# Optimization experiments

Hardware: AMD Instinct MI355X
Metric: run time of the kernel (lower is better)

## Reference

```python
import jax, jax.numpy as jnp
import numpy as np

B, N, FIN, HID, HEADS, LAYERS = 2048, 62, 128, 512, 8, 3
FOUT = HID // HEADS  # 64


def setup_inputs() -> dict:
    key = jax.random.key(0)
    ks = jax.random.split(key, 12)
    x = jax.random.normal(ks[0], (B, N, FIN), dtype=jnp.float32)
    adj = jax.random.randint(ks[1], (B, N, N), 0, 2, dtype=jnp.int32)
    # BatchNorm1d(62) params (eval mode, running stats)
    bn_gamma = jax.random.normal(ks[2], (N,), dtype=jnp.float32) * 0.1 + 1.0
    bn_beta = jax.random.normal(ks[3], (N,), dtype=jnp.float32) * 0.1
    bn_mean = jax.random.normal(ks[4], (N,), dtype=jnp.float32) * 0.1
    bn_var = jax.random.uniform(ks[5], (N,), dtype=jnp.float32, minval=0.5, maxval=1.5)
    # input MLP
    W_mlp = jax.random.normal(ks[6], (FIN, HID), dtype=jnp.float32) / np.sqrt(FIN)
    b_mlp = jnp.zeros((HID,), dtype=jnp.float32)
    # GAT params: one W [HID, FOUT] and one a [2*FOUT] per (layer, head)
    W_gat = jax.random.normal(ks[7], (LAYERS, HEADS, HID, FOUT), dtype=jnp.float32) / np.sqrt(HID)
    a_gat = jax.random.normal(ks[8], (LAYERS, HEADS, 2 * FOUT), dtype=jnp.float32) / np.sqrt(2 * FOUT)
    # output head
    W_out = jax.random.normal(ks[9], (HID, 3), dtype=jnp.float32) / np.sqrt(HID)
    b_out = jnp.zeros((3,), dtype=jnp.float32)
    return {
        "x": x, "adj": adj,
        "bn_gamma": bn_gamma, "bn_beta": bn_beta, "bn_mean": bn_mean, "bn_var": bn_var,
        "W_mlp": W_mlp, "b_mlp": b_mlp,
        "W_gat": W_gat, "a_gat": a_gat,
        "W_out": W_out, "b_out": b_out,
    }


def reference(x, adj, bn_gamma, bn_beta, bn_mean, bn_var, W_mlp, b_mlp, W_gat, a_gat, W_out, b_out):
    eps = 1e-5
    alpha = 0.2  # LeakyReLU slope
    # BatchNorm1d over the node dim (C=62), eval mode
    xb = (x - bn_mean[None, :, None]) * (bn_gamma / jnp.sqrt(bn_var + eps))[None, :, None] + bn_beta[None, :, None]
    h_x = xb @ W_mlp + b_mlp  # [B, N, HID]
    mask = adj > 0  # [B, N, N]
    n_layers, n_heads, _, f_out = W_gat.shape
    for l in range(n_layers):
        # all heads at once: h [H, B, N, FOUT]
        h = jnp.einsum('bnf,hfd->hbnd', h_x, W_gat[l])
        a1 = a_gat[l][:, :f_out]   # multiplies the repeat(1,N,1) part -> h_j
        a2 = a_gat[l][:, f_out:]   # multiplies the repeat(1,1,N) part -> h_i
        f1 = jnp.einsum('hbnd,hd->hbn', h, a1)  # per-node source term
        f2 = jnp.einsum('hbnd,hd->hbn', h, a2)  # per-node dest term
        # e[h,b,i,j] = leaky(a2.h_i + a1.h_j)  (matches cat/repeat layout)
        e = jax.nn.leaky_relu(f2[:, :, :, None] + f1[:, :, None, :], alpha)
        e = jnp.where(mask[None], e, jnp.float32(-9e15))
        # torch F.softmax(attention, dim=1) on [B,N,N] -> axis=2 here (the i axis)
        att = jax.nn.softmax(e, axis=2)
        hp = jnp.einsum('hbij,hbjd->hbid', att, h)
        hp = jax.nn.elu(hp)
        # concat heads on feature dim -> [B, N, HID]
        h_x = jnp.transpose(hp, (1, 2, 0, 3)).reshape(h_x.shape[0], h_x.shape[1], n_heads * f_out)
    pooled = jnp.sum(h_x, axis=1)  # [B, HID]
    logits = pooled @ W_out + b_out  # [B, 3]
    return jax.nn.log_softmax(logits, axis=-1)
```

## Files before the change

### kernel.cpp

```cpp
#include <hip/hip_runtime.h>
#include <cstdint>
#include <cstddef>

#define B_ 2048
#define N_ 62
#define FIN_ 128
#define HID_ 512
#define HEADS_ 8
#define FOUT_ 64
#define LAYERS_ 3
#define M_ (B_*N_)

typedef __bf16 bf16x8 __attribute__((ext_vector_type(8)));
typedef __bf16 bf16x4 __attribute__((ext_vector_type(4)));
typedef float  f32x4  __attribute__((ext_vector_type(4)));
typedef unsigned short u16;

#define LOG2E 1.4426950408889634f

#if __has_builtin(__builtin_amdgcn_exp2f)
#define EXP2F(x) __builtin_amdgcn_exp2f(x)
#else
#define EXP2F(x) exp2f(x)
#endif
#if __has_builtin(__builtin_amdgcn_logf)
#define LOG2F(x) __builtin_amdgcn_logf(x)
#else
#define LOG2F(x) log2f(x)
#endif

static __device__ __forceinline__ u16 f2bf(float f) {
    union { float f; uint32_t u; } v; v.f = f;
    uint32_t u = v.u;
    return (u16)((u + 0x7fffu + ((u >> 16) & 1u)) >> 16);
}
static __device__ __forceinline__ float bf2f(u16 s) {
    union { uint32_t u; float f; } v; v.u = ((uint32_t)s) << 16;
    return v.f;
}
static __device__ __forceinline__ float rdlane(float v, int l) {
    union { float f; int i; } a, b; a.f = v;
    b.i = __builtin_amdgcn_readlane(a.i, l);
    return b.f;
}
static __device__ __forceinline__ bf16x4 pack4(f32x4 v) {
    bf16x4 o;
    o[0] = (__bf16)v[0]; o[1] = (__bf16)v[1];
    o[2] = (__bf16)v[2]; o[3] = (__bf16)v[3];
    return o;
}

__global__ __launch_bounds__(256) void repack_w(
    const float* __restrict__ Wm, const float* __restrict__ Wg,
    u16* __restrict__ wmlp_t, u16* __restrict__ wgat2)
{
    int idx = blockIdx.x * 256 + threadIdx.x;
    const int T1 = HID_ * FIN_;
    const int T2 = LAYERS_ * HEADS_ * 64 * HID_;
    if (idx < T1) {
        int n = idx / FIN_, k = idx % FIN_;
        wmlp_t[idx] = f2bf(Wm[k * HID_ + n]);
    } else if (idx < T1 + T2) {
        int j = idx - T1;
        int lh = j / (64 * HID_);
        int r  = j % (64 * HID_);
        int n = r / HID_, k = r % HID_;
        wgat2[j] = f2bf(Wg[((size_t)lh * HID_ + k) * FOUT_ + n]);
    }
}

__global__ __launch_bounds__(256) void build_masks(
    const int* __restrict__ adj, uint64_t* __restrict__ masks,
    uint64_t* __restrict__ masksT)
{
    __shared__ uint32_t m32[128];
    const int b = blockIdx.x, tid = threadIdx.x;
    if (tid < 128) m32[tid] = 0;
    __syncthreads();
    const int* a = adj + (size_t)b * N_ * N_;
    for (int idx = tid; idx < N_ * N_; idx += 256) {
        int i = idx / N_, j = idx % N_;
        if (a[idx] > 0) atomicOr(&m32[i * 2 + (j >> 5)], 1u << (j & 31));
    }
    __syncthreads();
    if (tid < 128) ((uint32_t*)(masks + (size_t)b * 64))[tid] = m32[tid];
    if (tid < 64) {
        int j = tid;
        uint64_t c = 0;
        for (int i = 0; i < N_; i++) {
            uint64_t bit = (m32[i * 2 + (j >> 5)] >> (j & 31)) & 1u;
            c |= bit << i;
        }
        masksT[(size_t)b * 64 + j] = c;
    }
}

#define S_R  72
#define RSZ  4608
#define S_X  136
#define X0   27648

__global__ __launch_bounds__(512, 4) void gat_fused(
    const float* __restrict__ x,
    const float* __restrict__ bng, const float* __restrict__ bnb,
    const float* __restrict__ bnm, const float* __restrict__ bnv,
    const u16* __restrict__ wmlp_t, const float* __restrict__ bm,
    const u16* __restrict__ wgat2, const float* __restrict__ ag,
    const uint64_t* __restrict__ masks, const uint64_t* __restrict__ masksT,
    const float* __restrict__ Wout, const float* __restrict__ bout,
    float* __restrict__ out)
{
    __shared__ __align__(16) u16 buf[36864];
    __shared__ uint64_t msk[64];
    __shared__ __align__(16) float fstat[1544];
    float* F1 = fstat;
    float* F2 = fstat + 512;
    float* LS = fstat + 1024;

    const int tid = threadIdx.x, b = blockIdx.x;
    const int wave = tid >> 6, lane = tid & 63;
    const int lr = lane & 15, lq = lane >> 4;
    const int w64 = wave * 64;
    const int wreg = wave * RSZ;

    const uint64_t cm = masksT[(size_t)b * 64 + lane];
    const uint32_t cml = (uint32_t)cm, cmh = (uint32_t)(cm >> 32);

    {
        const float* xg = x + (size_t)b * N_ * FIN_;
        for (int idx = tid; idx < 2048; idx += 512) {
            int n = idx >> 5, kq = idx & 31;
            bf16x4 o = {(__bf16)0.f, (__bf16)0.f, (__bf16)0.f, (__bf16)0.f};
            if (n < N_) {
                float s = bng[n] * rsqrtf(bnv[n] + 1e-5f);
                float sh = bnb[n] - bnm[n] * s;
                float4 v = *(const float4*)(xg + n * FIN_ + kq * 4);
                o[0] = (__bf16)(v.x * s + sh); o[1] = (__bf16)(v.y * s + sh);
                o[2] = (__bf16)(v.z * s + sh); o[3] = (__bf16)(v.w * s + sh);
            }
            *(bf16x4*)&buf[X0 + n * S_X + kq * 4] = o;
        }
        if (tid < 64) msk[tid] = (tid < N_) ? masks[(size_t)b * 64 + tid] : 0ull;
    }
    __syncthreads();

    {
        f32x4 acc[4][4];
#pragma unroll
        for (int mt = 0; mt < 4; mt++)
#pragma unroll
            for (int nt = 0; nt < 4; nt++) acc[mt][nt] = (f32x4){0.f, 0.f, 0.f, 0.f};
        const int c0 = w64;
#pragma unroll 1
        for (int kt = 0; kt < 4; kt++) {
            int k0 = kt * 32;
            bf16x8 xf[4];
#pragma unroll
            for (int nt = 0; nt < 4; nt++)
                xf[nt] = *(const bf16x8*)&buf[X0 + (nt * 16 + lr) * S_X + k0 + lq * 8];
#pragma unroll
            for (int mt = 0; mt < 4; mt++) {
                bf16x8 wf = *(const bf16x8*)(wmlp_t + (size_t)(c0 + mt * 16 + lr) * FIN_ + k0 + lq * 8);
#pragma unroll
                for (int nt = 0; nt < 4; nt++)
                    acc[mt][nt] = __builtin_amdgcn_mfma_f32_16x16x32_bf16(
                        wf, xf[nt], acc[mt][nt], 0, 0, 0);
            }
        }
        __syncthreads();
        f32x4 bl[4];
#pragma unroll
        for (int mt = 0; mt < 4; mt++)
            bl[mt] = *(const f32x4*)&bm[c0 + mt * 16 + lq * 4];
#pragma unroll
        for (int mt = 0; mt < 4; mt++)
#pragma unroll
            for (int nt = 0; nt < 4; nt++) {
                int node = nt * 16 + lr;
                *(bf16x4*)&buf[wreg + node * S_R + mt * 16 + lq * 4] =
                    pack4(acc[mt][nt] + bl[mt]);
            }
        if (lane < 16) {
            uint4 z = {0u, 0u, 0u, 0u};
            *(uint4*)&buf[wreg + (N_ + (lane >> 3)) * S_R + (lane & 7) * 8] = z;
        }
    }
    __syncthreads();

#pragma unroll 1
    for (int l = 0; l < LAYERS_; l++) {
        const u16* wp = wgat2 + (size_t)(l * HEADS_ + wave) * 64 * HID_;

        f32x4 acc[4][4];
#pragma unroll
        for (int mt = 0; mt < 4; mt++)
#pragma unroll
            for (int nt = 0; nt < 4; nt++) acc[mt][nt] = (f32x4){0.f, 0.f, 0.f, 0.f};
#pragma unroll 1
        for (int kt = 0; kt < 16; kt++) {
            int koff = (kt >> 1) * RSZ + (kt & 1) * 32 + lq * 8;
            bf16x8 af[4];
#pragma unroll
            for (int mt = 0; mt < 4; mt++)
                af[mt] = *(const bf16x8*)&buf[koff + (mt * 16 + lr) * S_R];
#pragma unroll
            for (int nt = 0; nt < 4; nt++) {
                bf16x8 bfr = *(const bf16x8*)(wp + (size_t)(nt * 16 + lr) * HID_ + kt * 32 + lq * 8);
#pragma unroll
                for (int mt = 0; mt < 4; mt++)
                    acc[mt][nt] = __builtin_amdgcn_mfma_f32_16x16x32_bf16(
                        af[mt], bfr, acc[mt][nt], 0, 0, 0);
            }
        }

        {
            float a1v[4], a2v[4];
            const float* agl = ag + (size_t)(l * HEADS_ + wave) * 128;
#pragma unroll
            for (int nt = 0; nt < 4; nt++) {
                a1v[nt] = agl[nt * 16 + lr] * LOG2E;
                a2v[nt] = agl[64 + nt * 16 + lr] * LOG2E;
            }
            float p1v[16], p2v[16];
#pragma unroll
            for (int mt = 0; mt < 4; mt++)
#pragma unroll
                for (int r = 0; r < 4; r++) {
                    float s1 = 0.f, s2 = 0.f;
#pragma unroll
                    for (int nt = 0; nt < 4; nt++) {
                        float hv = acc[mt][nt][r];
                        s1 = fmaf(hv, a1v[nt], s1);
                        s2 = fmaf(hv, a2v[nt], s2);
                    }
                    p1v[mt * 4 + r] = s1;
                    p2v[mt * 4 + r] = s2;
                }
#pragma unroll
            for (int c = 0; c < 8; c++) {
                float tA = __shfl_xor(p1v[c], 8, 64);
                float tB = __shfl_xor(p1v[c + 8], 8, 64);
                p1v[c] = (lr & 8) ? (p1v[c + 8] + tB) : (p1v[c] + tA);
                float uA = __shfl_xor(p2v[c], 8, 64);
                float uB = __shfl_xor(p2v[c + 8], 8, 64);
                p2v[c] = (lr & 8) ? (p2v[c + 8] + uB) : (p2v[c] + uA);
            }
#pragma unroll
            for (int c = 0; c < 4; c++) {
                float tA = __shfl_xor(p1v[c], 4, 64);
                float tB = __shfl_xor(p1v[c + 4], 4, 64);
                p1v[c] = (lr & 4) ? (p1v[c + 4] + tB) : (p1v[c] + tA);
                float uA = __shfl_xor(p2v[c], 4, 64);
                float uB = __shfl_xor(p2v[c + 4], 4, 64);
                p2v[c] = (lr & 4) ? (p2v[c + 4] + uB) : (p2v[c] + uA);
            }
#pragma unroll
            for (int c = 0; c < 2; c++) {
                float tA = __shfl_xor(p1v[c], 2, 64);
                float tB = __shfl_xor(p1v[c + 2], 2, 64);
                p1v[c] = (lr & 2) ? (p1v[c + 2] + tB) : (p1v[c] + tA);
                float uA = __shfl_xor(p2v[c], 2, 64);
                float uB = __shfl_xor(p2v[c + 2], 2, 64);
                p2v[c] = (lr & 2) ? (p2v[c + 2] + uB) : (p2v[c] + uA);
            }
            {
                float tA = __shfl_xor(p1v[0], 1, 64);
                float tB = __shfl_xor(p1v[1], 1, 64);
                float f1fin = (lr & 1) ? (p1v[1] + tB) : (p1v[0] + tA);
                float uA = __shfl_xor(p2v[0], 1, 64);
                float uB = __shfl_xor(p2v[1], 1, 64);
                float f2fin = (lr & 1) ? (p2v[1] + uB) : (p2v[0] + uA);
                int node = (lr >> 2) * 16 + lq * 4 + (lr & 3);
                F1[w64 + node] = f1fin;
                F2[w64 + node] = f2fin;
            }
        }

        __syncthreads();

#pragma unroll
        for (int mt = 0; mt < 4; mt++)
#pragma unroll
            for (int nt = 0; nt < 4; nt++)
                *(bf16x4*)&buf[wreg + (nt * 16 + lr) * S_R + mt * 16 + lq * 4] =
                    pack4(acc[mt][nt]);

        float pm;
        {
            float p1 = F1[w64 + lane];
            float p2 = F2[w64 + lane];
            float t = (lane < N_) ? p2 : -3.0e38f;
#pragma unroll
            for (int off = 32; off; off >>= 1) t = fmaxf(t, __shfl_xor(t, off, 64));
            pm = t;
            float mprime = pm + p1;
            float m = fmaxf(mprime, 0.2f * mprime);
            float A  = EXP2F(p2 - pm);
            float C  = EXP2F(0.2f * (p2 - pm));
            float be = EXP2F(mprime - m);
            float de = EXP2F(0.2f * mprime - m);
            float s0 = 0.f, s1 = 0.f;
#pragma unroll
            for (int i = 0; i < N_; i += 2) {
                float aA = rdlane(A, i), aC = rdlane(C, i);
                float bA = rdlane(A, i + 1), bC = rdlane(C, i + 1);
                float ea = fmaxf(aA * be, aC * de);
                float eb = fmaxf(bA * be, bC * de);
                uint32_t w = (i < 32) ? cml : cmh;
                s0 += ((w >> (i & 31)) & 1u) ? ea : 0.f;
                s1 += ((w >> ((i + 1) & 31)) & 1u) ? eb : 0.f;
            }
            float ssum = fmaxf(s0 + s1, 1e-35f);
            float ls = m + LOG2F(ssum);
            F1[w64 + lane] = EXP2F(mprime - ls);
            LS[w64 + lane] = EXP2F(0.2f * mprime - ls);
        }

        f32x4 acc2[4][4];
#pragma unroll
        for (int mt = 0; mt < 4; mt++)
#pragma unroll
            for (int it = 0; it < 4; it++) acc2[mt][it] = (f32x4){0.f, 0.f, 0.f, 0.f};
        float A4[4], C4[4];
#pragma unroll
        for (int it = 0; it < 4; it++) {
            float f2 = F2[w64 + it * 16 + lr];
            A4[it] = EXP2F(f2 - pm);
            C4[it] = EXP2F(0.2f * (f2 - pm));
        }
#pragma unroll
        for (int kt = 0; kt < 2; kt++) {
            int j0 = kt * 32 + lq * 8;
            bf16x8 pf[4];
#pragma unroll
            for (int h = 0; h < 2; h++) {
                f32x4 bn = *(const f32x4*)&F1[w64 + j0 + 4 * h];
                f32x4 dn = *(const f32x4*)&LS[w64 + j0 + 4 * h];
#pragma unroll
                for (int it = 0; it < 4; it++) {
                    uint64_t mi = msk[it * 16 + lr];
                    uint32_t sh = ((uint32_t)(mi >> (kt * 32))) >> (lq * 8 + 4 * h);
#pragma unroll
                    for (int t = 0; t < 4; t++) {
                        float p = fmaxf(A4[it] * bn[t], C4[it] * dn[t]);
                        p = ((sh >> t) & 1u) ? p : 0.f;
                        pf[it][4 * h + t] = (__bf16)p;
                    }
                }
            }
#pragma unroll
            for (int mt = 0; mt < 4; mt++) {
                bf16x8 ha = *(const bf16x8*)&buf[wreg + (mt * 16 + lr) * S_R + kt * 32 + lq * 8];
#pragma unroll
                for (int it = 0; it < 4; it++)
                    acc2[mt][it] = __builtin_amdgcn_mfma_f32_16x16x32_bf16(
                        ha, pf[it], acc2[mt][it], 0, 0, 0);
            }
        }

#pragma unroll
        for (int mt = 0; mt < 4; mt++)
#pragma unroll
            for (int it = 0; it < 4; it++) {
                int i = it * 16 + lr;
                f32x4 e;
#pragma unroll
                for (int r = 0; r < 4; r++) {
                    float v = acc2[mt][it][r];
                    e[r] = v > 0.f ? v : EXP2F(v * LOG2E) - 1.f;
                }
                *(bf16x4*)&buf[wreg + i * S_R + mt * 16 + lq * 4] = pack4(e);
            }
        if (lane < 16) {
            uint4 z = {0u, 0u, 0u, 0u};
            *(uint4*)&buf[wreg + (N_ + (lane >> 3)) * S_R + (lane & 7) * 8] = z;
        }
        __syncthreads();
    }

    {
        float s = 0.f;
#pragma unroll 2
        for (int n = 0; n < N_; n++)
            s += bf2f(buf[(tid >> 6) * RSZ + n * S_R + (tid & 63)]);
        fstat[tid] = s;
    }
    __syncthreads();
    if (tid < 192) {
        int c = tid >> 6, ln = tid & 63;
        float p = 0.f;
#pragma unroll
        for (int k = ln; k < HID_; k += 64) p += fstat[k] * Wout[k * 3 + c];
        for (int off = 32; off > 0; off >>= 1) p += __shfl_down(p, off, 64);
        if (ln == 0) fstat[1536 + c] = p + bout[c];
    }
    __syncthreads();
    if (tid == 0) {
        float l0 = fstat[1536], l1 = fstat[1537], l2 = fstat[1538];
        float mm = fmaxf(l0, fmaxf(l1, l2));
        float s = __expf(l0 - mm) + __expf(l1 - mm) + __expf(l2 - mm);
        float ls = mm + logf(s);
        out[b * 3 + 0] = l0 - ls;
        out[b * 3 + 1] = l1 - ls;
        out[b * 3 + 2] = l2 - ls;
    }
}

extern "C" void kernel_launch(void* const* d_in, const int* in_sizes, int n_in,
                              void* d_out, int out_size, void* d_ws, size_t ws_size,
                              hipStream_t stream)
{
    const float* x   = (const float*)d_in[0];
    const int*   adj = (const int*)d_in[1];
    const float* bng = (const float*)d_in[2];
    const float* bnb = (const float*)d_in[3];
    const float* bnm = (const float*)d_in[4];
    const float* bnv = (const float*)d_in[5];
    const float* Wm  = (const float*)d_in[6];
    const float* bm  = (const float*)d_in[7];
    const float* Wg  = (const float*)d_in[8];
    const float* ag  = (const float*)d_in[9];
    const float* Wo  = (const float*)d_in[10];
    const float* bo  = (const float*)d_in[11];
    float* out = (float*)d_out;

    uint64_t* masks  = (uint64_t*)d_ws;
    uint64_t* masksT = masks + (size_t)B_ * 64;
    u16* wmlp_t = (u16*)(masksT + (size_t)B_ * 64);
    u16* wgat2  = wmlp_t + (size_t)HID_ * FIN_;

    int rep_total = HID_ * FIN_ + LAYERS_ * HEADS_ * 64 * HID_;
    repack_w<<<(rep_total + 255) / 256, 256, 0, stream>>>(Wm, Wg, wmlp_t, wgat2);
    build_masks<<<B_, 256, 0, stream>>>(adj, masks, masksT);

    gat_fused<<<B_, 512, 0, stream>>>(
        x, bng, bnb, bnm, bnv, wmlp_t, bm, wgat2, ag,
        masks, masksT, Wo, bo, out);
}
```

Baseline: 628.8 us.

## Fuse adjacency mask construction into main GAT kernel and derive A from C

```diff
diff --git a/kernel.cpp b/kernel.cpp
--- a/kernel.cpp
+++ b/kernel.cpp
@@ -69,44 +69,17 @@
     }
 }
 
-__global__ __launch_bounds__(256) void build_masks(
-    const int* __restrict__ adj, uint64_t* __restrict__ masks,
-    uint64_t* __restrict__ masksT)
-{
-    __shared__ uint32_t m32[128];
-    const int b = blockIdx.x, tid = threadIdx.x;
-    if (tid < 128) m32[tid] = 0;
-    __syncthreads();
-    const int* a = adj + (size_t)b * N_ * N_;
-    for (int idx = tid; idx < N_ * N_; idx += 256) {
-        int i = idx / N_, j = idx % N_;
-        if (a[idx] > 0) atomicOr(&m32[i * 2 + (j >> 5)], 1u << (j & 31));
-    }
-    __syncthreads();
-    if (tid < 128) ((uint32_t*)(masks + (size_t)b * 64))[tid] = m32[tid];
-    if (tid < 64) {
-        int j = tid;
-        uint64_t c = 0;
-        for (int i = 0; i < N_; i++) {
-            uint64_t bit = (m32[i * 2 + (j >> 5)] >> (j & 31)) & 1u;
-            c |= bit << i;
-        }
-        masksT[(size_t)b * 64 + j] = c;
-    }
-}
-
 #define S_R  72
 #define RSZ  4608
 #define S_X  136
 #define X0   27648
 
 __global__ __launch_bounds__(512, 4) void gat_fused(
-    const float* __restrict__ x,
+    const float* __restrict__ x, const int* __restrict__ adj,
     const float* __restrict__ bng, const float* __restrict__ bnb,
     const float* __restrict__ bnm, const float* __restrict__ bnv,
     const u16* __restrict__ wmlp_t, const float* __restrict__ bm,
     const u16* __restrict__ wgat2, const float* __restrict__ ag,
-    const uint64_t* __restrict__ masks, const uint64_t* __restrict__ masksT,
     const float* __restrict__ Wout, const float* __restrict__ bout,
     float* __restrict__ out)
 {
@@ -123,8 +96,16 @@
     const int w64 = wave * 64;
     const int wreg = wave * RSZ;
 
-    const uint64_t cm = masksT[(size_t)b * 64 + lane];
-    const uint32_t cml = (uint32_t)cm, cmh = (uint32_t)(cm >> 32);
+    {
+        const int* arow = adj + (size_t)b * N_ * N_;
+#pragma unroll
+        for (int rr = 0; rr < 8; rr++) {
+            int i = wave * 8 + rr;
+            int v = (i < N_ && lane < N_) ? arow[i * N_ + lane] : 0;
+            uint64_t bmask = __ballot(v > 0);
+            if (lane == 0) msk[i] = (i < N_) ? bmask : 0ull;
+        }
+    }
 
     {
         const float* xg = x + (size_t)b * N_ * FIN_;
@@ -140,9 +121,16 @@
             }
             *(bf16x4*)&buf[X0 + n * S_X + kq * 4] = o;
         }
-        if (tid < 64) msk[tid] = (tid < N_) ? masks[(size_t)b * 64 + tid] : 0ull;
     }
     __syncthreads();
+
+    uint32_t cml, cmh;
+    {
+        uint64_t cmv = 0;
+#pragma unroll
+        for (int i = 0; i < N_; i++) cmv |= ((msk[i] >> lane) & 1ull) << i;
+        cml = (uint32_t)cmv; cmh = (uint32_t)(cmv >> 32);
+    }
 
     {
         f32x4 acc[4][4];
@@ -285,14 +273,13 @@
                 *(bf16x4*)&buf[wreg + (nt * 16 + lr) * S_R + mt * 16 + lq * 4] =
                     pack4(acc[mt][nt]);
 
-        float pm;
         {
             float p1 = F1[w64 + lane];
             float p2 = F2[w64 + lane];
             float t = (lane < N_) ? p2 : -3.0e38f;
 #pragma unroll
             for (int off = 32; off; off >>= 1) t = fmaxf(t, __shfl_xor(t, off, 64));
-            pm = t;
+            float pm = t;
             float mprime = pm + p1;
             float m = fmaxf(mprime, 0.2f * mprime);
             float A  = EXP2F(p2 - pm);
@@ -314,6 +301,7 @@
             float ls = m + LOG2F(ssum);
             F1[w64 + lane] = EXP2F(mprime - ls);
             LS[w64 + lane] = EXP2F(0.2f * mprime - ls);
+            F2[w64 + lane] = C;
         }
 
         f32x4 acc2[4][4];
@@ -321,13 +309,6 @@
         for (int mt = 0; mt < 4; mt++)
 #pragma unroll
             for (int it = 0; it < 4; it++) acc2[mt][it] = (f32x4){0.f, 0.f, 0.f, 0.f};
-        float A4[4], C4[4];
-#pragma unroll
-        for (int it = 0; it < 4; it++) {
-            float f2 = F2[w64 + it * 16 + lr];
-            A4[it] = EXP2F(f2 - pm);
-            C4[it] = EXP2F(0.2f * (f2 - pm));
-        }
 #pragma unroll
         for (int kt = 0; kt < 2; kt++) {
             int j0 = kt * 32 + lq * 8;
@@ -338,11 +319,14 @@
                 f32x4 dn = *(const f32x4*)&LS[w64 + j0 + 4 * h];
 #pragma unroll
                 for (int it = 0; it < 4; it++) {
+                    float Cv = F2[w64 + it * 16 + lr];
+                    float c2 = Cv * Cv;
+                    float Av = c2 * c2 * Cv;
                     uint64_t mi = msk[it * 16 + lr];
                     uint32_t sh = ((uint32_t)(mi >> (kt * 32))) >> (lq * 8 + 4 * h);
 #pragma unroll
                     for (int t = 0; t < 4; t++) {
-                        float p = fmaxf(A4[it] * bn[t], C4[it] * dn[t]);
+                        float p = fmaxf(Av * bn[t], Cv * dn[t]);
                         p = ((sh >> t) & 1u) ? p : 0.f;
                         pf[it][4 * h + t] = (__bf16)p;
                     }
@@ -424,16 +408,13 @@
     const float* bo  = (const float*)d_in[11];
     float* out = (float*)d_out;
 
-    uint64_t* masks  = (uint64_t*)d_ws;
-    uint64_t* masksT = masks + (size_t)B_ * 64;
-    u16* wmlp_t = (u16*)(masksT + (size_t)B_ * 64);
+    u16* wmlp_t = (u16*)d_ws;
     u16* wgat2  = wmlp_t + (size_t)HID_ * FIN_;
 
     int rep_total = HID_ * FIN_ + LAYERS_ * HEADS_ * 64 * HID_;
     repack_w<<<(rep_total + 255) / 256, 256, 0, stream>>>(Wm, Wg, wmlp_t, wgat2);
-    build_masks<<<B_, 256, 0, stream>>>(adj, masks, masksT);
 
     gat_fused<<<B_, 512, 0, stream>>>(
-        x, bng, bnb, bnm, bnv, wmlp_t, bm, wgat2, ag,
-        masks, masksT, Wo, bo, out);
-}
+        x, adj, bng, bnb, bnm, bnv, wmlp_t, bm, wgat2, ag,
+        Wo, bo, out);
+}
```

New measurement: 735.2 us. 16.9% more time.
